# Optimization experiments

Hardware: AMD Instinct MI355X
Metric: run time of the kernel (lower is better)

Reference implementation:

```python
import jax, jax.numpy as jnp
import numpy as np

B, L, T = 256, 1024, 128

def setup_inputs() -> dict:
    key = jax.random.key(0)
    k1, k2, k3, k4 = jax.random.split(key, 4)
    inputs = jax.random.normal(k1, (B, L, T), dtype=jnp.float32)
    tag_indices = jax.random.randint(k2, (B, L), 0, T, dtype=jnp.int64)
    sequence_lengths = jax.random.randint(k3, (B,), 1, L + 1, dtype=jnp.int64)
    # xavier-ish scale for transitions
    transition_params = jax.random.normal(k4, (T, T), dtype=jnp.float32) * (2.0 / (T + T)) ** 0.5
    return {"inputs": inputs, "tag_indices": tag_indices,
            "sequence_lengths": sequence_lengths, "transition_params": transition_params}

def _crf_log_likelihood(inputs, tag_indices, sequence_lengths, transition_params):
    b, l, t = inputs.shape
    mask = (jnp.arange(l)[None, :] < sequence_lengths[:, None]).astype(inputs.dtype)  # [B,L]

    # --- unary score: sum_t inputs[b, t, tag[b,t]] over valid t ---
    unary = jnp.take_along_axis(inputs, tag_indices[:, :, None], axis=2)[:, :, 0]  # [B,L]
    unary_score = jnp.sum(unary * mask, axis=1)

    # --- binary score: sum_t trans[tag[t], tag[t+1]] masked by mask[:,1:] ---
    trans_sc = transition_params[tag_indices[:, :-1], tag_indices[:, 1:]]  # [B,L-1]
    binary_score = jnp.sum(trans_sc * mask[:, 1:], axis=1)
    sequence_scores = unary_score + binary_score

    # --- log normalizer via forward algorithm (log-space scan) ---
    first = inputs[:, 0]                               # [B,T]
    rest = jnp.transpose(inputs[:, 1:], (1, 0, 2))     # [L-1,B,T]

    def step(state, inp_t):
        # state: [B,T] previous alphas; transition broadcast: [B,T_prev,T_next]
        new = inp_t + jax.nn.logsumexp(state[:, :, None] + transition_params[None], axis=1)
        return new, new

    _, alphas = jax.lax.scan(step, first, rest)        # [L-1,B,T]
    # original indexes all_alphas at max(0, seq_len - 2)
    idx = jnp.clip(sequence_lengths - 2, 0, l - 2)
    final_alphas = alphas[idx, jnp.arange(b)]          # [B,T]
    log_norm = jax.nn.logsumexp(final_alphas, axis=1)
    log_norm = jnp.where(sequence_lengths <= 0, jnp.zeros_like(log_norm), log_norm)

    return sequence_scores - log_norm

def reference(inputs, tag_indices, sequence_lengths, transition_params):
    return _crf_log_likelihood(inputs, tag_indices, sequence_lengths, transition_params)
```

## Files before the change

kernel.cpp:

```cpp
#include <hip/hip_runtime.h>


#define B_   256
#define LL   1024
#define TT   128
#define NBLK 16
#define L2E  1.4426950408889634f
#define LN2f 0.6931471805599453f

typedef __attribute__((ext_vector_type(8))) short bf16x8;
typedef __attribute__((ext_vector_type(4))) float f32x4;
union bfrw { unsigned w[4]; bf16x8 v; };

__device__ __forceinline__ unsigned bfround(float x) {
    unsigned u = __float_as_uint(x);
    return u + 0x7fffu + ((u >> 16) & 1u);
}
__device__ __forceinline__ unsigned pack2(float lo, float hi) {
#if __has_builtin(__builtin_amdgcn_cvt_pk_bf16_f32)
    auto p = __builtin_amdgcn_cvt_pk_bf16_f32(lo, hi);
    unsigned w; __builtin_memcpy(&w, &p, 4); return w;
#else
    return __builtin_amdgcn_perm(bfround(hi), bfround(lo), 0x07060302);
#endif
}
__device__ __forceinline__ void lds_barrier() {
    asm volatile("s_waitcnt lgkmcnt(0)\n\ts_barrier" ::: "memory");
}

template<bool FWD, int PH>
__device__ __forceinline__ void phase(int t, float& Dacc, float4 (&up)[4][2],
                                      const bf16x8 (&af)[2][4],
                                      short* qls, float* sb, const float* pu,
                                      float* __restrict__ qcap, float* __restrict__ rcap,
                                      float* __restrict__ dqv, float* __restrict__ drv,
                                      int cb, int tfin, int rank,
                                      int wid, int quad, int bl)
{
    constexpr int CUR  = PH & 1;
    constexpr int NXT  = CUR ^ 1;
    constexpr int SLOT = FWD ? ((1 + PH) & 3) : ((3 - PH) & 3);

    bfrw bfr[4];
    #pragma unroll
    for (int c = 0; c < 4; ++c)
        bfr[c].v = *(const bf16x8*)(qls + CUR * (16 * 136) + bl * 136 + (4 * c + quad) * 8);
    float sprev = sb[CUR * 16 + bl];
    float ci = __builtin_amdgcn_rcpf(sprev);

    f32x4 ae0 = {0.f,0.f,0.f,0.f}, ao0 = {0.f,0.f,0.f,0.f};
    f32x4 ae1 = {0.f,0.f,0.f,0.f}, ao1 = {0.f,0.f,0.f,0.f};
    ae0 = __builtin_amdgcn_mfma_f32_16x16x32_bf16(af[0][0], bfr[0].v, ae0, 0, 0, 0);
    ae1 = __builtin_amdgcn_mfma_f32_16x16x32_bf16(af[1][0], bfr[0].v, ae1, 0, 0, 0);
    ao0 = __builtin_amdgcn_mfma_f32_16x16x32_bf16(af[0][1], bfr[1].v, ao0, 0, 0, 0);
    ao1 = __builtin_amdgcn_mfma_f32_16x16x32_bf16(af[1][1], bfr[1].v, ao1, 0, 0, 0);
    ae0 = __builtin_amdgcn_mfma_f32_16x16x32_bf16(af[0][2], bfr[2].v, ae0, 0, 0, 0);
    ae1 = __builtin_amdgcn_mfma_f32_16x16x32_bf16(af[1][2], bfr[2].v, ae1, 0, 0, 0);
    ao0 = __builtin_amdgcn_mfma_f32_16x16x32_bf16(af[0][3], bfr[3].v, ao0, 0, 0, 0);
    ao1 = __builtin_amdgcn_mfma_f32_16x16x32_bf16(af[1][3], bfr[3].v, ao1, 0, 0, 0);

    float ex[8];
    #pragma unroll
    for (int mt = 0; mt < 2; ++mt) {
        float4 v = up[SLOT][mt];
        ex[4*mt+0] = __builtin_amdgcn_exp2f(v.x * L2E);
        ex[4*mt+1] = __builtin_amdgcn_exp2f(v.y * L2E);
        ex[4*mt+2] = __builtin_amdgcn_exp2f(v.z * L2E);
        ex[4*mt+3] = __builtin_amdgcn_exp2f(v.w * L2E);
    }
    {
        int tp = FWD ? (t + 4) : (t - 5);
        tp = tp < 0 ? 0 : (tp > LL - 1 ? LL - 1 : tp);
        #pragma unroll
        for (int mt = 0; mt < 2; ++mt)
            up[SLOT][mt] = *(const float4*)(pu + (size_t)tp * TT + mt * 16);
    }
    Dacc += __builtin_amdgcn_logf(sprev);

    f32x4 s0v = ae0 + ao0;
    f32x4 s1v = ae1 + ao1;

    float rv[8];
    #pragma unroll
    for (int r = 0; r < 4; ++r) { rv[r] = ci * s0v[r]; rv[4 + r] = ci * s1v[r]; }

    if (!FWD) {
        bool cap = (cb == t - 1) && (cb != tfin);
        if (__any(cap)) {
            if (cap) {
                float4 c0 = {rv[0], rv[1], rv[2], rv[3]};
                float4 c1 = {rv[4], rv[5], rv[6], rv[7]};
                *(float4*)(rcap + rank * TT + wid * 32 + quad * 4) = c0;
                *(float4*)(rcap + rank * TT + wid * 32 + 16 + quad * 4) = c1;
                if (wid == 0 && quad == 0) drv[rank] = Dacc;
            }
        }
        bool inj = (tfin == t - 1);
        #pragma unroll
        for (int k = 0; k < 8; ++k) rv[k] = inj ? 1.0f : rv[k];
        Dacc = inj ? 0.0f : Dacc;
    }

    float ov[8];
    #pragma unroll
    for (int k = 0; k < 8; ++k) ov[k] = ex[k] * rv[k];

    if (FWD) {
        bool cap = (cb == t);
        if (__any(cap)) {
            if (cap) {
                float4 c0 = {ov[0], ov[1], ov[2], ov[3]};
                float4 c1 = {ov[4], ov[5], ov[6], ov[7]};
                *(float4*)(qcap + rank * TT + wid * 32 + quad * 4) = c0;
                *(float4*)(qcap + rank * TT + wid * 32 + 16 + quad * 4) = c1;
                if (wid == 0 && quad == 0) dqv[rank] = Dacc;
            }
        }
    }

    if (wid == 0 && quad == 0) sb[NXT * 16 + bl] = s0v[0];

    bfrw pk;
    pk.w[0] = pack2(ov[0], ov[1]);
    pk.w[1] = pack2(ov[2], ov[3]);
    pk.w[2] = pack2(ov[4], ov[5]);
    pk.w[3] = pack2(ov[6], ov[7]);
    *(bf16x8*)(qls + NXT * (16 * 136) + bl * 136 + (4 * wid + quad) * 8) = pk.v;

    lds_barrier();
}

__launch_bounds__(256, 1)
__global__ void crf_scan(const float* __restrict__ inputs,
                         const int*   __restrict__ tags,
                         const int*   __restrict__ slens,
                         const float* __restrict__ trans,
                         float* __restrict__ qcap, float* __restrict__ rcap,
                         float* __restrict__ dqv,  float* __restrict__ drv,
                         int* __restrict__ perm, float* __restrict__ scorebuf)
{
    __shared__ __align__(16) short qls[2 * 16 * 136];
    __shared__ float sb[2 * 16];
    __shared__ int keys[B_];

    const int tid  = threadIdx.x;

    if (blockIdx.x >= 2 * NBLK) {
        const int sbid = blockIdx.x - 2 * NBLK;
        const int lane = tid & 63, wid = tid >> 6;
        #pragma unroll 1
        for (int bi = 0; bi < 4; ++bi) {
            const int b = sbid * 4 + bi;
            const int slen = slens[b];
            const float* inb  = inputs + (size_t)b * LL * TT;
            const int*   tagb = tags + b * LL;
            float sc = 0.f;
            for (int t = tid; t < slen; t += 256) {
                int tg = tagb[t];
                float v = inb[(size_t)t * TT + tg];
                if (t >= 1) v += trans[tagb[t - 1] * TT + tg];
                sc += v;
            }
            #pragma unroll
            for (int off = 32; off > 0; off >>= 1) sc += __shfl_xor(sc, off, 64);
            if (lane == 0) sb[wid] = sc;
            __syncthreads();
            if (tid == 0) scorebuf[b] = sb[0] + sb[1] + sb[2] + sb[3];
            __syncthreads();
        }
        return;
    }

    const int lane = tid & 63;
    const int wid  = __builtin_amdgcn_readfirstlane(tid >> 6);
    const int quad = lane >> 4;
    const int bl   = lane & 15;
    const bool isf = (blockIdx.x < NBLK);
    const int g    = isf ? blockIdx.x : blockIdx.x - NBLK;

    keys[tid] = slens[tid] * 256 + tid;
    __syncthreads();
    for (int k = 2; k <= B_; k <<= 1) {
        for (int s = k >> 1; s > 0; s >>= 1) {
            int ixj = tid ^ s;
            if (ixj > tid) {
                int a = keys[tid], b2 = keys[ixj];
                bool asc = ((tid & k) == 0);
                if ((a > b2) == asc) { keys[tid] = b2; keys[ixj] = a; }
            }
            __syncthreads();
        }
    }
    if (isf && tid < 16) perm[g * 16 + tid] = keys[g * 16 + tid] & 255;

    const int key = keys[g * 16 + bl];
    const int ob  = key & 255;
    const int sl  = key >> 8;
    int tfin = sl - 1; if (tfin < 1) tfin = 1;

    int tmax = tfin;
    #pragma unroll
    for (int o = 1; o < 16; o <<= 1) {
        int c2 = __shfl_xor(tmax, o, 16); tmax = c2 > tmax ? c2 : tmax;
    }
    tmax = __builtin_amdgcn_readfirstlane(tmax);

    const int C  = (tmax + 4) >> 1;
    const int cb = tfin < C ? tfin : C;

    int cmax = cb, cmin = cb;
    #pragma unroll
    for (int o = 1; o < 16; o <<= 1) {
        int a = __shfl_xor(cmax, o, 16); cmax = a > cmax ? a : cmax;
        int b2 = __shfl_xor(cmin, o, 16); cmin = b2 < cmin ? b2 : cmin;
    }
    cmax = __builtin_amdgcn_readfirstlane(cmax);
    cmin = __builtin_amdgcn_readfirstlane(cmin);

    bf16x8 af[2][4];
    #pragma unroll
    for (int mt = 0; mt < 2; ++mt) {
        const int j = wid * 32 + mt * 16 + bl;
        #pragma unroll
        for (int c = 0; c < 4; ++c) {
            #pragma unroll
            for (int jj = 0; jj < 8; ++jj) {
                int k = 32 * c + 16 * (jj >> 2) + 4 * quad + (jj & 3);
                int idx = isf ? (k * TT + j) : (j * TT + k);
                float ev = __builtin_amdgcn_exp2f(trans[idx] * L2E);
                af[mt][c][jj] = (short)(bfround(ev) >> 16);
            }
        }
    }

    const float* pu = inputs + (size_t)ob * LL * TT + wid * 32 + quad * 4;
    const int rank = g * 16 + bl;
    float Dacc = 0.f;
    float4 up[4][2];

    if (tid < 16) sb[tid] = 1.0f;

    if (isf) {
        float q0[8];
        #pragma unroll
        for (int mt = 0; mt < 2; ++mt) {
            float4 v = *(const float4*)(pu + mt * 16);
            q0[4*mt+0] = __builtin_amdgcn_exp2f(v.x * L2E);
            q0[4*mt+1] = __builtin_amdgcn_exp2f(v.y * L2E);
            q0[4*mt+2] = __builtin_amdgcn_exp2f(v.z * L2E);
            q0[4*mt+3] = __builtin_amdgcn_exp2f(v.w * L2E);
        }
        bfrw pk;
        pk.w[0] = pack2(q0[0], q0[1]);
        pk.w[1] = pack2(q0[2], q0[3]);
        pk.w[2] = pack2(q0[4], q0[5]);
        pk.w[3] = pack2(q0[6], q0[7]);
        *(bf16x8*)(qls + bl * 136 + (4 * wid + quad) * 8) = pk.v;

        #pragma unroll
        for (int s = 1; s <= 4; ++s) {
            #pragma unroll
            for (int mt = 0; mt < 2; ++mt)
                up[s & 3][mt] = *(const float4*)(pu + (size_t)s * TT + mt * 16);
        }
        __syncthreads();

        for (int tb = 1; tb <= cmax; tb += 4) {
            phase<true,0>(tb+0, Dacc, up, af, qls, sb, pu, qcap, rcap, dqv, drv, cb, tfin, rank, wid, quad, bl);
            phase<true,1>(tb+1, Dacc, up, af, qls, sb, pu, qcap, rcap, dqv, drv, cb, tfin, rank, wid, quad, bl);
            phase<true,2>(tb+2, Dacc, up, af, qls, sb, pu, qcap, rcap, dqv, drv, cb, tfin, rank, wid, quad, bl);
            phase<true,3>(tb+3, Dacc, up, af, qls, sb, pu, qcap, rcap, dqv, drv, cb, tfin, rank, wid, quad, bl);
        }
    } else {
        bfrw pk;
        pk.w[0] = pk.w[1] = pk.w[2] = pk.w[3] = 0x3F803F80u;
        *(bf16x8*)(qls + bl * 136 + (4 * wid + quad) * 8) = pk.v;
        if (cb == tfin) {
            float4 one4 = {1.f, 1.f, 1.f, 1.f};
            *(float4*)(rcap + rank * TT + wid * 32 + quad * 4) = one4;
            *(float4*)(rcap + rank * TT + wid * 32 + 16 + quad * 4) = one4;
            if (wid == 0 && quad == 0) drv[rank] = 0.f;
        }

        const int tb0 = (tmax + 4) & ~3;
        #pragma unroll
        for (int ph = 0; ph < 4; ++ph) {
            int ui = tb0 - 1 - ph;
            ui = ui > LL - 1 ? LL - 1 : (ui < 0 ? 0 : ui);
            #pragma unroll
            for (int mt = 0; mt < 2; ++mt)
                up[(3 - ph) & 3][mt] = *(const float4*)(pu + (size_t)ui * TT + mt * 16);
        }
        __syncthreads();

        for (int tb = tb0; tb > cmin; tb -= 4) {
            phase<false,0>(tb-0, Dacc, up, af, qls, sb, pu, qcap, rcap, dqv, drv, cb, tfin, rank, wid, quad, bl);
            phase<false,1>(tb-1, Dacc, up, af, qls, sb, pu, qcap, rcap, dqv, drv, cb, tfin, rank, wid, quad, bl);
            phase<false,2>(tb-2, Dacc, up, af, qls, sb, pu, qcap, rcap, dqv, drv, cb, tfin, rank, wid, quad, bl);
            phase<false,3>(tb-3, Dacc, up, af, qls, sb, pu, qcap, rcap, dqv, drv, cb, tfin, rank, wid, quad, bl);
        }
    }
}

__global__ void crf_comb(const float* __restrict__ qcap, const float* __restrict__ rcap,
                         const float* __restrict__ dqv, const float* __restrict__ drv,
                         const int* __restrict__ perm, const float* __restrict__ scorebuf,
                         float* __restrict__ out) {
    const int tid = threadIdx.x;
    const int r16 = tid >> 4, part = tid & 15;
    const int rank = blockIdx.x * 16 + r16;
    const float* qc = qcap + rank * TT + part * 8;
    const float* rc = rcap + rank * TT + part * 8;
    float4 a0 = *(const float4*)(qc);
    float4 a1 = *(const float4*)(qc + 4);
    float4 b0 = *(const float4*)(rc);
    float4 b1 = *(const float4*)(rc + 4);
    float s = a0.x*b0.x + a0.y*b0.y + a0.z*b0.z + a0.w*b0.w
            + a1.x*b1.x + a1.y*b1.y + a1.z*b1.z + a1.w*b1.w;
    #pragma unroll
    for (int o = 1; o < 16; o <<= 1) s += __shfl_xor(s, o, 16);
    if (part == 0) {
        int ob = perm[rank];
        float logZ = LN2f * (__builtin_amdgcn_logf(s) + dqv[rank] + drv[rank]);
        out[ob] = scorebuf[ob] - logZ;
    }
}

extern "C" void kernel_launch(void* const* d_in, const int* in_sizes, int n_in,
                              void* d_out, int out_size, void* d_ws, size_t ws_size,
                              hipStream_t stream) {
    const float* inputs = (const float*)d_in[0];
    const int*   tags   = (const int*)d_in[1];
    const int*   slens  = (const int*)d_in[2];
    const float* trans  = (const float*)d_in[3];
    float* out = (float*)d_out;

    float* qcap = (float*)d_ws;
    float* rcap = qcap + 32768;
    float* dqv  = rcap + 32768;
    float* drv  = dqv + 256;
    int*   perm = (int*)(drv + 256);
    float* scorebuf = (float*)(perm + 256);

    crf_scan<<<2 * NBLK + 64, 256, 0, stream>>>(inputs, tags, slens, trans,
                                                qcap, rcap, dqv, drv, perm, scorebuf);
    crf_comb<<<NBLK, 256, 0, stream>>>(qcap, rcap, dqv, drv, perm, scorebuf, out);
}
```

Measured before the change: 410.3 us.

## Run each CRF scan block on a single wavefront with register-resident state

Each forward/backward scan block now runs on one 64-lane wavefront instead of four. That wave computes all 128 output tags, using 8 MFMA tiles per K-chunk. The packed bf16 MFMA outputs are fed straight back as the next step's B operand, and the per-sequence scale is broadcast with ds_bpermute. This removes the per-step LDS write/read and the block barrier. In exchange, each wave issues four times as many MFMAs serially and holds much larger register arrays (transition fragments and the prefetch ring). Captured vectors go into LDS and are copied to global memory once at the end.

```diff
diff --git a/kernel.cpp b/kernel.cpp
--- a/kernel.cpp
+++ b/kernel.cpp
@@ -24,110 +24,115 @@
     return __builtin_amdgcn_perm(bfround(hi), bfround(lo), 0x07060302);
 #endif
 }
-__device__ __forceinline__ void lds_barrier() {
-    asm volatile("s_waitcnt lgkmcnt(0)\n\ts_barrier" ::: "memory");
-}
 
 template<bool FWD, int PH>
-__device__ __forceinline__ void phase(int t, float& Dacc, float4 (&up)[4][2],
-                                      const bf16x8 (&af)[2][4],
-                                      short* qls, float* sb, const float* pu,
-                                      float* __restrict__ qcap, float* __restrict__ rcap,
-                                      float* __restrict__ dqv, float* __restrict__ drv,
-                                      int cb, int tfin, int rank,
-                                      int wid, int quad, int bl)
+__device__ __forceinline__ void phase1(int t, float& Dacc, float& sprev,
+                                       float4 (&up)[4][8],
+                                       const bf16x8 (&af)[8][4],
+                                       bf16x8 (&bfr)[4],
+                                       const float* pu,
+                                       float* capl, float* dcap,
+                                       int cb, int tfin, int q, int b)
 {
-    constexpr int CUR  = PH & 1;
-    constexpr int NXT  = CUR ^ 1;
     constexpr int SLOT = FWD ? ((1 + PH) & 3) : ((3 - PH) & 3);
 
-    bfrw bfr[4];
-    #pragma unroll
-    for (int c = 0; c < 4; ++c)
-        bfr[c].v = *(const bf16x8*)(qls + CUR * (16 * 136) + bl * 136 + (4 * c + quad) * 8);
-    float sprev = sb[CUR * 16 + bl];
-    float ci = __builtin_amdgcn_rcpf(sprev);
-
-    f32x4 ae0 = {0.f,0.f,0.f,0.f}, ao0 = {0.f,0.f,0.f,0.f};
-    f32x4 ae1 = {0.f,0.f,0.f,0.f}, ao1 = {0.f,0.f,0.f,0.f};
-    ae0 = __builtin_amdgcn_mfma_f32_16x16x32_bf16(af[0][0], bfr[0].v, ae0, 0, 0, 0);
-    ae1 = __builtin_amdgcn_mfma_f32_16x16x32_bf16(af[1][0], bfr[0].v, ae1, 0, 0, 0);
-    ao0 = __builtin_amdgcn_mfma_f32_16x16x32_bf16(af[0][1], bfr[1].v, ao0, 0, 0, 0);
-    ao1 = __builtin_amdgcn_mfma_f32_16x16x32_bf16(af[1][1], bfr[1].v, ao1, 0, 0, 0);
-    ae0 = __builtin_amdgcn_mfma_f32_16x16x32_bf16(af[0][2], bfr[2].v, ae0, 0, 0, 0);
-    ae1 = __builtin_amdgcn_mfma_f32_16x16x32_bf16(af[1][2], bfr[2].v, ae1, 0, 0, 0);
-    ao0 = __builtin_amdgcn_mfma_f32_16x16x32_bf16(af[0][3], bfr[3].v, ao0, 0, 0, 0);
-    ao1 = __builtin_amdgcn_mfma_f32_16x16x32_bf16(af[1][3], bfr[3].v, ao1, 0, 0, 0);
-
-    float ex[8];
-    #pragma unroll
-    for (int mt = 0; mt < 2; ++mt) {
+    f32x4 acc[8];
+    #pragma unroll
+    for (int mt = 0; mt < 8; ++mt)
+        acc[mt] = __builtin_amdgcn_mfma_f32_16x16x32_bf16(
+            af[mt][0], bfr[0], (f32x4){0.f, 0.f, 0.f, 0.f}, 0, 0, 0);
+    #pragma unroll
+    for (int c = 1; c < 4; ++c) {
+        #pragma unroll
+        for (int mt = 0; mt < 8; ++mt)
+            acc[mt] = __builtin_amdgcn_mfma_f32_16x16x32_bf16(
+                af[mt][c], bfr[c], acc[mt], 0, 0, 0);
+    }
+
+    float ex[8][4];
+    #pragma unroll
+    for (int mt = 0; mt < 8; ++mt) {
         float4 v = up[SLOT][mt];
-        ex[4*mt+0] = __builtin_amdgcn_exp2f(v.x * L2E);
-        ex[4*mt+1] = __builtin_amdgcn_exp2f(v.y * L2E);
-        ex[4*mt+2] = __builtin_amdgcn_exp2f(v.z * L2E);
-        ex[4*mt+3] = __builtin_amdgcn_exp2f(v.w * L2E);
+        ex[mt][0] = __builtin_amdgcn_exp2f(v.x * L2E);
+        ex[mt][1] = __builtin_amdgcn_exp2f(v.y * L2E);
+        ex[mt][2] = __builtin_amdgcn_exp2f(v.z * L2E);
+        ex[mt][3] = __builtin_amdgcn_exp2f(v.w * L2E);
     }
     {
         int tp = FWD ? (t + 4) : (t - 5);
         tp = tp < 0 ? 0 : (tp > LL - 1 ? LL - 1 : tp);
-        #pragma unroll
-        for (int mt = 0; mt < 2; ++mt)
-            up[SLOT][mt] = *(const float4*)(pu + (size_t)tp * TT + mt * 16);
-    }
-    Dacc += __builtin_amdgcn_logf(sprev);
-
-    f32x4 s0v = ae0 + ao0;
-    f32x4 s1v = ae1 + ao1;
-
-    float rv[8];
-    #pragma unroll
-    for (int r = 0; r < 4; ++r) { rv[r] = ci * s0v[r]; rv[4 + r] = ci * s1v[r]; }
+        const float* pt = pu + (size_t)tp * TT;
+        #pragma unroll
+        for (int mt = 0; mt < 8; ++mt)
+            up[SLOT][mt] = *(const float4*)(pt + mt * 16);
+    }
+
+    float ci = __builtin_amdgcn_rcpf(sprev);
+    float lg = __builtin_amdgcn_logf(sprev);
+    bool inj = (!FWD) && (tfin == t - 1);
+    float cis  = inj ? 0.f : ci;
+    float injf = inj ? 1.f : 0.f;
+    Dacc = inj ? 0.f : (Dacc + lg);
+
+    float rv[8][4];
+    #pragma unroll
+    for (int mt = 0; mt < 8; ++mt) {
+        #pragma unroll
+        for (int r = 0; r < 4; ++r)
+            rv[mt][r] = cis * acc[mt][r] + injf;
+    }
 
     if (!FWD) {
         bool cap = (cb == t - 1) && (cb != tfin);
         if (__any(cap)) {
             if (cap) {
-                float4 c0 = {rv[0], rv[1], rv[2], rv[3]};
-                float4 c1 = {rv[4], rv[5], rv[6], rv[7]};
-                *(float4*)(rcap + rank * TT + wid * 32 + quad * 4) = c0;
-                *(float4*)(rcap + rank * TT + wid * 32 + 16 + quad * 4) = c1;
-                if (wid == 0 && quad == 0) drv[rank] = Dacc;
-            }
-        }
-        bool inj = (tfin == t - 1);
-        #pragma unroll
-        for (int k = 0; k < 8; ++k) rv[k] = inj ? 1.0f : rv[k];
-        Dacc = inj ? 0.0f : Dacc;
-    }
-
-    float ov[8];
-    #pragma unroll
-    for (int k = 0; k < 8; ++k) ov[k] = ex[k] * rv[k];
+                #pragma unroll
+                for (int mt = 0; mt < 8; ++mt) {
+                    float4 c4 = {rv[mt][0], rv[mt][1], rv[mt][2], rv[mt][3]};
+                    *(float4*)(capl + b * TT + mt * 16 + q * 4) = c4;
+                }
+                if (q == 0) dcap[b] = Dacc;
+            }
+        }
+    }
+
+    float ov[8][4];
+    #pragma unroll
+    for (int mt = 0; mt < 8; ++mt) {
+        #pragma unroll
+        for (int r = 0; r < 4; ++r)
+            ov[mt][r] = ex[mt][r] * rv[mt][r];
+    }
 
     if (FWD) {
         bool cap = (cb == t);
         if (__any(cap)) {
             if (cap) {
-                float4 c0 = {ov[0], ov[1], ov[2], ov[3]};
-                float4 c1 = {ov[4], ov[5], ov[6], ov[7]};
-                *(float4*)(qcap + rank * TT + wid * 32 + quad * 4) = c0;
-                *(float4*)(qcap + rank * TT + wid * 32 + 16 + quad * 4) = c1;
-                if (wid == 0 && quad == 0) dqv[rank] = Dacc;
-            }
-        }
-    }
-
-    if (wid == 0 && quad == 0) sb[NXT * 16 + bl] = s0v[0];
-
-    bfrw pk;
-    pk.w[0] = pack2(ov[0], ov[1]);
-    pk.w[1] = pack2(ov[2], ov[3]);
-    pk.w[2] = pack2(ov[4], ov[5]);
-    pk.w[3] = pack2(ov[6], ov[7]);
-    *(bf16x8*)(qls + NXT * (16 * 136) + bl * 136 + (4 * wid + quad) * 8) = pk.v;
-
-    lds_barrier();
+                #pragma unroll
+                for (int mt = 0; mt < 8; ++mt) {
+                    float4 c4 = {ov[mt][0], ov[mt][1], ov[mt][2], ov[mt][3]};
+                    *(float4*)(capl + b * TT + mt * 16 + q * 4) = c4;
+                }
+                if (q == 0) dcap[b] = Dacc;
+            }
+        }
+    }
+
+    {
+        int s0i = __float_as_int(acc[0][0]);
+        int sp  = __builtin_amdgcn_ds_bpermute(b << 2, s0i);
+        sprev = __int_as_float(sp);
+    }
+
+    #pragma unroll
+    for (int c = 0; c < 4; ++c) {
+        bfrw pk;
+        pk.w[0] = pack2(ov[2*c][0],     ov[2*c][1]);
+        pk.w[1] = pack2(ov[2*c][2],     ov[2*c][3]);
+        pk.w[2] = pack2(ov[2*c+1][0],   ov[2*c+1][1]);
+        pk.w[3] = pack2(ov[2*c+1][2],   ov[2*c+1][3]);
+        bfr[c] = pk.v;
+    }
 }
 
 __launch_bounds__(256, 1)
@@ -139,11 +144,12 @@
                          float* __restrict__ dqv,  float* __restrict__ drv,
                          int* __restrict__ perm, float* __restrict__ scorebuf)
 {
-    __shared__ __align__(16) short qls[2 * 16 * 136];
+    __shared__ __align__(16) float capl[16 * TT];
+    __shared__ float dcap[16];
     __shared__ float sb[2 * 16];
     __shared__ int keys[B_];
 
-    const int tid  = threadIdx.x;
+    const int tid = threadIdx.x;
 
     if (blockIdx.x >= 2 * NBLK) {
         const int sbid = blockIdx.x - 2 * NBLK;
@@ -171,13 +177,6 @@
         return;
     }
 
-    const int lane = tid & 63;
-    const int wid  = __builtin_amdgcn_readfirstlane(tid >> 6);
-    const int quad = lane >> 4;
-    const int bl   = lane & 15;
-    const bool isf = (blockIdx.x < NBLK);
-    const int g    = isf ? blockIdx.x : blockIdx.x - NBLK;
-
     keys[tid] = slens[tid] * 256 + tid;
     __syncthreads();
     for (int k = 2; k <= B_; k <<= 1) {
@@ -191,9 +190,17 @@
             __syncthreads();
         }
     }
+
+    const bool isf = (blockIdx.x < NBLK);
+    const int g    = isf ? blockIdx.x : blockIdx.x - NBLK;
     if (isf && tid < 16) perm[g * 16 + tid] = keys[g * 16 + tid] & 255;
 
-    const int key = keys[g * 16 + bl];
+    if (tid >= 64) return;
+
+    const int q = tid >> 4;
+    const int b = tid & 15;
+
+    const int key = keys[g * 16 + b];
     const int ob  = key & 255;
     const int sl  = key >> 8;
     int tfin = sl - 1; if (tfin < 1) tfin = 1;
@@ -217,15 +224,15 @@
     cmax = __builtin_amdgcn_readfirstlane(cmax);
     cmin = __builtin_amdgcn_readfirstlane(cmin);
 
-    bf16x8 af[2][4];
-    #pragma unroll
-    for (int mt = 0; mt < 2; ++mt) {
-        const int j = wid * 32 + mt * 16 + bl;
+    bf16x8 af[8][4];
+    #pragma unroll
+    for (int mt = 0; mt < 8; ++mt) {
+        const int j = 16 * mt + b;
         #pragma unroll
         for (int c = 0; c < 4; ++c) {
             #pragma unroll
             for (int jj = 0; jj < 8; ++jj) {
-                int k = 32 * c + 16 * (jj >> 2) + 4 * quad + (jj & 3);
+                int k = 32 * c + 16 * (jj >> 2) + 4 * q + (jj & 3);
                 int idx = isf ? (k * TT + j) : (j * TT + k);
                 float ev = __builtin_amdgcn_exp2f(trans[idx] * L2E);
                 af[mt][c][jj] = (short)(bfround(ev) >> 16);
@@ -233,53 +240,57 @@
         }
     }
 
-    const float* pu = inputs + (size_t)ob * LL * TT + wid * 32 + quad * 4;
-    const int rank = g * 16 + bl;
-    float Dacc = 0.f;
-    float4 up[4][2];
-
-    if (tid < 16) sb[tid] = 1.0f;
+    const float* pu = inputs + (size_t)ob * LL * TT + q * 4;
+    float Dacc = 0.f, sprev = 1.0f;
+    float4 up[4][8];
+    bf16x8 bfr[4];
 
     if (isf) {
-        float q0[8];
-        #pragma unroll
-        for (int mt = 0; mt < 2; ++mt) {
+        float q0[8][4];
+        #pragma unroll
+        for (int mt = 0; mt < 8; ++mt) {
             float4 v = *(const float4*)(pu + mt * 16);
-            q0[4*mt+0] = __builtin_amdgcn_exp2f(v.x * L2E);
-            q0[4*mt+1] = __builtin_amdgcn_exp2f(v.y * L2E);
-            q0[4*mt+2] = __builtin_amdgcn_exp2f(v.z * L2E);
-            q0[4*mt+3] = __builtin_amdgcn_exp2f(v.w * L2E);
-        }
-        bfrw pk;
-        pk.w[0] = pack2(q0[0], q0[1]);
-        pk.w[1] = pack2(q0[2], q0[3]);
-        pk.w[2] = pack2(q0[4], q0[5]);
-        pk.w[3] = pack2(q0[6], q0[7]);
-        *(bf16x8*)(qls + bl * 136 + (4 * wid + quad) * 8) = pk.v;
-
+            q0[mt][0] = __builtin_amdgcn_exp2f(v.x * L2E);
+            q0[mt][1] = __builtin_amdgcn_exp2f(v.y * L2E);
+            q0[mt][2] = __builtin_amdgcn_exp2f(v.z * L2E);
+            q0[mt][3] = __builtin_amdgcn_exp2f(v.w * L2E);
+        }
+        #pragma unroll
+        for (int c = 0; c < 4; ++c) {
+            bfrw pk;
+            pk.w[0] = pack2(q0[2*c][0],   q0[2*c][1]);
+            pk.w[1] = pack2(q0[2*c][2],   q0[2*c][3]);
+            pk.w[2] = pack2(q0[2*c+1][0], q0[2*c+1][1]);
+            pk.w[3] = pack2(q0[2*c+1][2], q0[2*c+1][3]);
+            bfr[c] = pk.v;
+        }
         #pragma unroll
         for (int s = 1; s <= 4; ++s) {
-            #pragma unroll
-            for (int mt = 0; mt < 2; ++mt)
-                up[s & 3][mt] = *(const float4*)(pu + (size_t)s * TT + mt * 16);
-        }
-        __syncthreads();
+            int tp = s > LL - 1 ? LL - 1 : s;
+            #pragma unroll
+            for (int mt = 0; mt < 8; ++mt)
+                up[s & 3][mt] = *(const float4*)(pu + (size_t)tp * TT + mt * 16);
+        }
 
         for (int tb = 1; tb <= cmax; tb += 4) {
-            phase<true,0>(tb+0, Dacc, up, af, qls, sb, pu, qcap, rcap, dqv, drv, cb, tfin, rank, wid, quad, bl);
-            phase<true,1>(tb+1, Dacc, up, af, qls, sb, pu, qcap, rcap, dqv, drv, cb, tfin, rank, wid, quad, bl);
-            phase<true,2>(tb+2, Dacc, up, af, qls, sb, pu, qcap, rcap, dqv, drv, cb, tfin, rank, wid, quad, bl);
-            phase<true,3>(tb+3, Dacc, up, af, qls, sb, pu, qcap, rcap, dqv, drv, cb, tfin, rank, wid, quad, bl);
+            phase1<true,0>(tb+0, Dacc, sprev, up, af, bfr, pu, capl, dcap, cb, tfin, q, b);
+            phase1<true,1>(tb+1, Dacc, sprev, up, af, bfr, pu, capl, dcap, cb, tfin, q, b);
+            phase1<true,2>(tb+2, Dacc, sprev, up, af, bfr, pu, capl, dcap, cb, tfin, q, b);
+            phase1<true,3>(tb+3, Dacc, sprev, up, af, bfr, pu, capl, dcap, cb, tfin, q, b);
         }
     } else {
-        bfrw pk;
-        pk.w[0] = pk.w[1] = pk.w[2] = pk.w[3] = 0x3F803F80u;
-        *(bf16x8*)(qls + bl * 136 + (4 * wid + quad) * 8) = pk.v;
+        {
+            bfrw pk;
+            pk.w[0] = pk.w[1] = pk.w[2] = pk.w[3] = 0x3F803F80u;
+            #pragma unroll
+            for (int c = 0; c < 4; ++c) bfr[c] = pk.v;
+        }
         if (cb == tfin) {
             float4 one4 = {1.f, 1.f, 1.f, 1.f};
-            *(float4*)(rcap + rank * TT + wid * 32 + quad * 4) = one4;
-            *(float4*)(rcap + rank * TT + wid * 32 + 16 + quad * 4) = one4;
-            if (wid == 0 && quad == 0) drv[rank] = 0.f;
+            #pragma unroll
+            for (int mt = 0; mt < 8; ++mt)
+                *(float4*)(capl + b * TT + mt * 16 + q * 4) = one4;
+            if (q == 0) dcap[b] = 0.f;
         }
 
         const int tb0 = (tmax + 4) & ~3;
@@ -288,18 +299,26 @@
             int ui = tb0 - 1 - ph;
             ui = ui > LL - 1 ? LL - 1 : (ui < 0 ? 0 : ui);
             #pragma unroll
-            for (int mt = 0; mt < 2; ++mt)
+            for (int mt = 0; mt < 8; ++mt)
                 up[(3 - ph) & 3][mt] = *(const float4*)(pu + (size_t)ui * TT + mt * 16);
         }
-        __syncthreads();
 
         for (int tb = tb0; tb > cmin; tb -= 4) {
-            phase<false,0>(tb-0, Dacc, up, af, qls, sb, pu, qcap, rcap, dqv, drv, cb, tfin, rank, wid, quad, bl);
-            phase<false,1>(tb-1, Dacc, up, af, qls, sb, pu, qcap, rcap, dqv, drv, cb, tfin, rank, wid, quad, bl);
-            phase<false,2>(tb-2, Dacc, up, af, qls, sb, pu, qcap, rcap, dqv, drv, cb, tfin, rank, wid, quad, bl);
-            phase<false,3>(tb-3, Dacc, up, af, qls, sb, pu, qcap, rcap, dqv, drv, cb, tfin, rank, wid, quad, bl);
-        }
-    }
+            phase1<false,0>(tb-0, Dacc, sprev, up, af, bfr, pu, capl, dcap, cb, tfin, q, b);
+            phase1<false,1>(tb-1, Dacc, sprev, up, af, bfr, pu, capl, dcap, cb, tfin, q, b);
+            phase1<false,2>(tb-2, Dacc, sprev, up, af, bfr, pu, capl, dcap, cb, tfin, q, b);
+            phase1<false,3>(tb-3, Dacc, sprev, up, af, bfr, pu, capl, dcap, cb, tfin, q, b);
+        }
+    }
+
+    asm volatile("s_waitcnt lgkmcnt(0)" ::: "memory");
+    float* gout = isf ? qcap : rcap;
+    #pragma unroll
+    for (int i = 0; i < 8; ++i) {
+        float4 v = *(const float4*)(capl + i * 256 + tid * 4);
+        *(float4*)(gout + (size_t)g * 16 * TT + i * 256 + tid * 4) = v;
+    }
+    if (tid < 16) (isf ? dqv : drv)[g * 16 + tid] = dcap[tid];
 }
 
 __global__ void crf_comb(const float* __restrict__ qcap, const float* __restrict__ rcap,
```

After: 612.1 us. 1.49x slower.

## Merge forward and backward scans into one 512-thread block with register-reused fragments

Applied to the files above, without the earlier changes.

Forward and backward chains for the same 16 sequences now run in one 512-thread block, each half with its own LDS buffers, which halves the scan grid. Each wave keeps its own bf16 B-fragment in registers and reads only the other three from LDS in a fragment-major layout, cutting LDS traffic per step. Captures are staged in LDS and written out at the end, and the backward injection branch becomes arithmetic. Both halves loop for the larger of the two trip counts and share block barriers, so the shorter direction does extra steps.

```diff
diff --git a/kernel.cpp b/kernel.cpp
--- a/kernel.cpp
+++ b/kernel.cpp
@@ -28,109 +28,118 @@
     asm volatile("s_waitcnt lgkmcnt(0)\n\ts_barrier" ::: "memory");
 }
 
+
 template<bool FWD, int PH>
-__device__ __forceinline__ void phase(int t, float& Dacc, float4 (&up)[4][2],
+__device__ __forceinline__ void phase(int t, float& Dacc,
+                                      float4 (&up)[4][2],
                                       const bf16x8 (&af)[2][4],
-                                      short* qls, float* sb, const float* pu,
-                                      float* __restrict__ qcap, float* __restrict__ rcap,
-                                      float* __restrict__ dqv, float* __restrict__ drv,
-                                      int cb, int tfin, int rank,
-                                      int wid, int quad, int bl)
+                                      bf16x8& bs,
+                                      short* fset, float* sb2,
+                                      const float* pu,
+                                      float* cl, float* dc,
+                                      int o0, int o1, int o2, int ws,
+                                      int cb, int tfin, int W4, int q, int b)
 {
     constexpr int CUR  = PH & 1;
     constexpr int NXT  = CUR ^ 1;
     constexpr int SLOT = FWD ? ((1 + PH) & 3) : ((3 - PH) & 3);
 
-    bfrw bfr[4];
-    #pragma unroll
-    for (int c = 0; c < 4; ++c)
-        bfr[c].v = *(const bf16x8*)(qls + CUR * (16 * 136) + bl * 136 + (4 * c + quad) * 8);
-    float sprev = sb[CUR * 16 + bl];
-    float ci = __builtin_amdgcn_rcpf(sprev);
-
-    f32x4 ae0 = {0.f,0.f,0.f,0.f}, ao0 = {0.f,0.f,0.f,0.f};
-    f32x4 ae1 = {0.f,0.f,0.f,0.f}, ao1 = {0.f,0.f,0.f,0.f};
-    ae0 = __builtin_amdgcn_mfma_f32_16x16x32_bf16(af[0][0], bfr[0].v, ae0, 0, 0, 0);
-    ae1 = __builtin_amdgcn_mfma_f32_16x16x32_bf16(af[1][0], bfr[0].v, ae1, 0, 0, 0);
-    ao0 = __builtin_amdgcn_mfma_f32_16x16x32_bf16(af[0][1], bfr[1].v, ao0, 0, 0, 0);
-    ao1 = __builtin_amdgcn_mfma_f32_16x16x32_bf16(af[1][1], bfr[1].v, ao1, 0, 0, 0);
-    ae0 = __builtin_amdgcn_mfma_f32_16x16x32_bf16(af[0][2], bfr[2].v, ae0, 0, 0, 0);
-    ae1 = __builtin_amdgcn_mfma_f32_16x16x32_bf16(af[1][2], bfr[2].v, ae1, 0, 0, 0);
-    ao0 = __builtin_amdgcn_mfma_f32_16x16x32_bf16(af[0][3], bfr[3].v, ao0, 0, 0, 0);
-    ao1 = __builtin_amdgcn_mfma_f32_16x16x32_bf16(af[1][3], bfr[3].v, ao1, 0, 0, 0);
-
-    float ex[8];
-    #pragma unroll
-    for (int mt = 0; mt < 2; ++mt) {
-        float4 v = up[SLOT][mt];
-        ex[4*mt+0] = __builtin_amdgcn_exp2f(v.x * L2E);
-        ex[4*mt+1] = __builtin_amdgcn_exp2f(v.y * L2E);
-        ex[4*mt+2] = __builtin_amdgcn_exp2f(v.z * L2E);
-        ex[4*mt+3] = __builtin_amdgcn_exp2f(v.w * L2E);
+    bf16x8 bo0 = *(const bf16x8*)(fset + CUR * 2048 + o0);
+    bf16x8 bo1 = *(const bf16x8*)(fset + CUR * 2048 + o1);
+    bf16x8 bo2 = *(const bf16x8*)(fset + CUR * 2048 + o2);
+    float sprev = sb2[CUR * 16 + b];
+
+    f32x4 ae0, ae1, ao0, ao1;
+    ae0 = __builtin_amdgcn_mfma_f32_16x16x32_bf16(af[0][0], bs,  (f32x4){0.f,0.f,0.f,0.f}, 0, 0, 0);
+    ae1 = __builtin_amdgcn_mfma_f32_16x16x32_bf16(af[1][0], bs,  (f32x4){0.f,0.f,0.f,0.f}, 0, 0, 0);
+    ao0 = __builtin_amdgcn_mfma_f32_16x16x32_bf16(af[0][1], bo0, (f32x4){0.f,0.f,0.f,0.f}, 0, 0, 0);
+    ao1 = __builtin_amdgcn_mfma_f32_16x16x32_bf16(af[1][1], bo0, (f32x4){0.f,0.f,0.f,0.f}, 0, 0, 0);
+    ae0 = __builtin_amdgcn_mfma_f32_16x16x32_bf16(af[0][2], bo1, ae0, 0, 0, 0);
+    ae1 = __builtin_amdgcn_mfma_f32_16x16x32_bf16(af[1][2], bo1, ae1, 0, 0, 0);
+    ao0 = __builtin_amdgcn_mfma_f32_16x16x32_bf16(af[0][3], bo2, ao0, 0, 0, 0);
+    ao1 = __builtin_amdgcn_mfma_f32_16x16x32_bf16(af[1][3], bo2, ao1, 0, 0, 0);
+
+    float ex[2][4];
+    #pragma unroll
+    for (int m = 0; m < 2; ++m) {
+        float4 v = up[SLOT][m];
+        ex[m][0] = __builtin_amdgcn_exp2f(v.x * L2E);
+        ex[m][1] = __builtin_amdgcn_exp2f(v.y * L2E);
+        ex[m][2] = __builtin_amdgcn_exp2f(v.z * L2E);
+        ex[m][3] = __builtin_amdgcn_exp2f(v.w * L2E);
     }
     {
         int tp = FWD ? (t + 4) : (t - 5);
         tp = tp < 0 ? 0 : (tp > LL - 1 ? LL - 1 : tp);
-        #pragma unroll
-        for (int mt = 0; mt < 2; ++mt)
-            up[SLOT][mt] = *(const float4*)(pu + (size_t)tp * TT + mt * 16);
-    }
-    Dacc += __builtin_amdgcn_logf(sprev);
-
-    f32x4 s0v = ae0 + ao0;
-    f32x4 s1v = ae1 + ao1;
-
-    float rv[8];
-    #pragma unroll
-    for (int r = 0; r < 4; ++r) { rv[r] = ci * s0v[r]; rv[4 + r] = ci * s1v[r]; }
+        const float* pt = pu + (size_t)tp * TT;
+        up[SLOT][0] = *(const float4*)(pt);
+        up[SLOT][1] = *(const float4*)(pt + 16);
+    }
+
+    float ci = __builtin_amdgcn_rcpf(sprev);
+    float lg = __builtin_amdgcn_logf(sprev);
+    bool inj = (!FWD) && (tfin == t - 1);
+    float cis  = inj ? 0.f : ci;
+    float injf = inj ? 1.f : 0.f;
+    Dacc = inj ? 0.f : (Dacc + lg);
+
+    f32x4 a0 = ae0 + ao0;
+    f32x4 a1 = ae1 + ao1;
+
+    float rv[2][4];
+    #pragma unroll
+    for (int r = 0; r < 4; ++r) {
+        rv[0][r] = cis * a0[r] + injf;
+        rv[1][r] = cis * a1[r] + injf;
+    }
 
     if (!FWD) {
         bool cap = (cb == t - 1) && (cb != tfin);
         if (__any(cap)) {
             if (cap) {
-                float4 c0 = {rv[0], rv[1], rv[2], rv[3]};
-                float4 c1 = {rv[4], rv[5], rv[6], rv[7]};
-                *(float4*)(rcap + rank * TT + wid * 32 + quad * 4) = c0;
-                *(float4*)(rcap + rank * TT + wid * 32 + 16 + quad * 4) = c1;
-                if (wid == 0 && quad == 0) drv[rank] = Dacc;
-            }
-        }
-        bool inj = (tfin == t - 1);
-        #pragma unroll
-        for (int k = 0; k < 8; ++k) rv[k] = inj ? 1.0f : rv[k];
-        Dacc = inj ? 0.0f : Dacc;
-    }
-
-    float ov[8];
-    #pragma unroll
-    for (int k = 0; k < 8; ++k) ov[k] = ex[k] * rv[k];
+                float4 c0 = {rv[0][0], rv[0][1], rv[0][2], rv[0][3]};
+                float4 c1 = {rv[1][0], rv[1][1], rv[1][2], rv[1][3]};
+                *(float4*)(cl + b * TT + 32 * W4 + q * 4)      = c0;
+                *(float4*)(cl + b * TT + 32 * W4 + 16 + q * 4) = c1;
+                if (W4 == 0 && q == 0) dc[b] = Dacc;
+            }
+        }
+    }
+
+    float ov[2][4];
+    #pragma unroll
+    for (int r = 0; r < 4; ++r) {
+        ov[0][r] = ex[0][r] * rv[0][r];
+        ov[1][r] = ex[1][r] * rv[1][r];
+    }
 
     if (FWD) {
         bool cap = (cb == t);
         if (__any(cap)) {
             if (cap) {
-                float4 c0 = {ov[0], ov[1], ov[2], ov[3]};
-                float4 c1 = {ov[4], ov[5], ov[6], ov[7]};
-                *(float4*)(qcap + rank * TT + wid * 32 + quad * 4) = c0;
-                *(float4*)(qcap + rank * TT + wid * 32 + 16 + quad * 4) = c1;
-                if (wid == 0 && quad == 0) dqv[rank] = Dacc;
-            }
-        }
-    }
-
-    if (wid == 0 && quad == 0) sb[NXT * 16 + bl] = s0v[0];
+                float4 c0 = {ov[0][0], ov[0][1], ov[0][2], ov[0][3]};
+                float4 c1 = {ov[1][0], ov[1][1], ov[1][2], ov[1][3]};
+                *(float4*)(cl + b * TT + 32 * W4 + q * 4)      = c0;
+                *(float4*)(cl + b * TT + 32 * W4 + 16 + q * 4) = c1;
+                if (W4 == 0 && q == 0) dc[b] = Dacc;
+            }
+        }
+    }
+
+    if (W4 == 0 && q == 0) sb2[NXT * 16 + b] = a0[0];
 
     bfrw pk;
-    pk.w[0] = pack2(ov[0], ov[1]);
-    pk.w[1] = pack2(ov[2], ov[3]);
-    pk.w[2] = pack2(ov[4], ov[5]);
-    pk.w[3] = pack2(ov[6], ov[7]);
-    *(bf16x8*)(qls + NXT * (16 * 136) + bl * 136 + (4 * wid + quad) * 8) = pk.v;
+    pk.w[0] = pack2(ov[0][0], ov[0][1]);
+    pk.w[1] = pack2(ov[0][2], ov[0][3]);
+    pk.w[2] = pack2(ov[1][0], ov[1][1]);
+    pk.w[3] = pack2(ov[1][2], ov[1][3]);
+    bs = pk.v;
+    *(bf16x8*)(fset + NXT * 2048 + ws) = pk.v;
 
     lds_barrier();
 }
 
-__launch_bounds__(256, 1)
+__launch_bounds__(512, 1)
 __global__ void crf_scan(const float* __restrict__ inputs,
                          const int*   __restrict__ tags,
                          const int*   __restrict__ slens,
@@ -139,15 +148,18 @@
                          float* __restrict__ dqv,  float* __restrict__ drv,
                          int* __restrict__ perm, float* __restrict__ scorebuf)
 {
-    __shared__ __align__(16) short qls[2 * 16 * 136];
-    __shared__ float sb[2 * 16];
+    __shared__ __align__(16) short fragls[2][2][4][64 * 8];
+    __shared__ __align__(16) float capl[2][16][TT];
+    __shared__ float dcap[2][16];
+    __shared__ float sbuf[2][2][16];
+    __shared__ float ssb[8];
     __shared__ int keys[B_];
 
-    const int tid  = threadIdx.x;
-
-    if (blockIdx.x >= 2 * NBLK) {
-        const int sbid = blockIdx.x - 2 * NBLK;
-        const int lane = tid & 63, wid = tid >> 6;
+    const int tid = threadIdx.x;
+
+    if (blockIdx.x >= NBLK) {
+        const int sbid = blockIdx.x - NBLK;
+        const int lane = tid & 63, w = tid >> 6;
         #pragma unroll 1
         for (int bi = 0; bi < 4; ++bi) {
             const int b = sbid * 4 + bi;
@@ -155,7 +167,7 @@
             const float* inb  = inputs + (size_t)b * LL * TT;
             const int*   tagb = tags + b * LL;
             float sc = 0.f;
-            for (int t = tid; t < slen; t += 256) {
+            for (int t = tid; t < slen; t += 512) {
                 int tg = tagb[t];
                 float v = inb[(size_t)t * TT + tg];
                 if (t >= 1) v += trans[tagb[t - 1] * TT + tg];
@@ -163,37 +175,42 @@
             }
             #pragma unroll
             for (int off = 32; off > 0; off >>= 1) sc += __shfl_xor(sc, off, 64);
-            if (lane == 0) sb[wid] = sc;
+            if (lane == 0) ssb[w] = sc;
             __syncthreads();
-            if (tid == 0) scorebuf[b] = sb[0] + sb[1] + sb[2] + sb[3];
+            if (tid == 0) scorebuf[b] = ssb[0] + ssb[1] + ssb[2] + ssb[3]
+                                      + ssb[4] + ssb[5] + ssb[6] + ssb[7];
             __syncthreads();
         }
         return;
     }
 
-    const int lane = tid & 63;
-    const int wid  = __builtin_amdgcn_readfirstlane(tid >> 6);
-    const int quad = lane >> 4;
-    const int bl   = lane & 15;
-    const bool isf = (blockIdx.x < NBLK);
-    const int g    = isf ? blockIdx.x : blockIdx.x - NBLK;
-
-    keys[tid] = slens[tid] * 256 + tid;
+    const int g = blockIdx.x;
+
+    if (tid < 256) keys[tid] = slens[tid] * 256 + tid;
     __syncthreads();
     for (int k = 2; k <= B_; k <<= 1) {
         for (int s = k >> 1; s > 0; s >>= 1) {
-            int ixj = tid ^ s;
-            if (ixj > tid) {
-                int a = keys[tid], b2 = keys[ixj];
-                bool asc = ((tid & k) == 0);
-                if ((a > b2) == asc) { keys[tid] = b2; keys[ixj] = a; }
+            if (tid < 256) {
+                int ixj = tid ^ s;
+                if (ixj > tid) {
+                    int a = keys[tid], b2 = keys[ixj];
+                    bool asc = ((tid & k) == 0);
+                    if ((a > b2) == asc) { keys[tid] = b2; keys[ixj] = a; }
+                }
             }
             __syncthreads();
         }
     }
-    if (isf && tid < 16) perm[g * 16 + tid] = keys[g * 16 + tid] & 255;
-
-    const int key = keys[g * 16 + bl];
+    if (tid < 16) perm[g * 16 + tid] = keys[g * 16 + tid] & 255;
+
+    const int set  = tid >> 8;
+    const bool isf = (set == 0);
+    const int lane = tid & 63;
+    const int W4   = __builtin_amdgcn_readfirstlane((tid >> 6) & 3);
+    const int q    = lane >> 4;
+    const int b    = lane & 15;
+
+    const int key = keys[g * 16 + b];
     const int ob  = key & 255;
     const int sl  = key >> 8;
     int tfin = sl - 1; if (tfin < 1) tfin = 1;
@@ -217,89 +234,118 @@
     cmax = __builtin_amdgcn_readfirstlane(cmax);
     cmin = __builtin_amdgcn_readfirstlane(cmin);
 
+    const int tb0 = (tmax + 4) & ~3;
+    const int nif = (cmax + 3) >> 2;
+    const int nib = (tb0 - cmin + 3) >> 2;
+    const int NS  = nif > nib ? nif : nib;
+
+    const int c1 = (W4 == 0) ? 1 : 0;
+    const int c2 = (W4 <= 1) ? 2 : 1;
+    const int c3 = (W4 <= 2) ? 3 : 2;
+    const int o0 = (c1 * 64 + lane) * 8;
+    const int o1 = (c2 * 64 + lane) * 8;
+    const int o2 = (c3 * 64 + lane) * 8;
+    const int ws = (W4 * 64 + lane) * 8;
+
     bf16x8 af[2][4];
     #pragma unroll
-    for (int mt = 0; mt < 2; ++mt) {
-        const int j = wid * 32 + mt * 16 + bl;
+    for (int m = 0; m < 2; ++m) {
+        const int j = 32 * W4 + 16 * m + b;
         #pragma unroll
-        for (int c = 0; c < 4; ++c) {
+        for (int i = 0; i < 4; ++i) {
+            const int c = (i == 0) ? W4 : (i == 1) ? c1 : (i == 2) ? c2 : c3;
             #pragma unroll
             for (int jj = 0; jj < 8; ++jj) {
-                int k = 32 * c + 16 * (jj >> 2) + 4 * quad + (jj & 3);
+                int k = 32 * c + 16 * (jj >> 2) + 4 * q + (jj & 3);
                 int idx = isf ? (k * TT + j) : (j * TT + k);
                 float ev = __builtin_amdgcn_exp2f(trans[idx] * L2E);
-                af[mt][c][jj] = (short)(bfround(ev) >> 16);
-            }
-        }
-    }
-
-    const float* pu = inputs + (size_t)ob * LL * TT + wid * 32 + quad * 4;
-    const int rank = g * 16 + bl;
+                af[m][i][jj] = (short)(bfround(ev) >> 16);
+            }
+        }
+    }
+
+    short* fset = &fragls[set][0][0][0];
+    float* sb2  = &sbuf[set][0][0];
+    float* cl   = &capl[set][0][0];
+    float* dc   = &dcap[set][0];
+
+    const float* pu = inputs + (size_t)ob * LL * TT + 32 * W4 + q * 4;
     float Dacc = 0.f;
     float4 up[4][2];
-
-    if (tid < 16) sb[tid] = 1.0f;
+    bf16x8 bs;
+
+    if (W4 == 0 && lane < 16) sb2[lane] = 1.0f;
 
     if (isf) {
-        float q0[8];
+        float q0[2][4];
         #pragma unroll
-        for (int mt = 0; mt < 2; ++mt) {
-            float4 v = *(const float4*)(pu + mt * 16);
-            q0[4*mt+0] = __builtin_amdgcn_exp2f(v.x * L2E);
-            q0[4*mt+1] = __builtin_amdgcn_exp2f(v.y * L2E);
-            q0[4*mt+2] = __builtin_amdgcn_exp2f(v.z * L2E);
-            q0[4*mt+3] = __builtin_amdgcn_exp2f(v.w * L2E);
+        for (int m = 0; m < 2; ++m) {
+            float4 v = *(const float4*)(pu + m * 16);
+            q0[m][0] = __builtin_amdgcn_exp2f(v.x * L2E);
+            q0[m][1] = __builtin_amdgcn_exp2f(v.y * L2E);
+            q0[m][2] = __builtin_amdgcn_exp2f(v.z * L2E);
+            q0[m][3] = __builtin_amdgcn_exp2f(v.w * L2E);
         }
         bfrw pk;
-        pk.w[0] = pack2(q0[0], q0[1]);
-        pk.w[1] = pack2(q0[2], q0[3]);
-        pk.w[2] = pack2(q0[4], q0[5]);
-        pk.w[3] = pack2(q0[6], q0[7]);
-        *(bf16x8*)(qls + bl * 136 + (4 * wid + quad) * 8) = pk.v;
+        pk.w[0] = pack2(q0[0][0], q0[0][1]);
+        pk.w[1] = pack2(q0[0][2], q0[0][3]);
+        pk.w[2] = pack2(q0[1][0], q0[1][1]);
+        pk.w[3] = pack2(q0[1][2], q0[1][3]);
+        bs = pk.v;
+        *(bf16x8*)(fset + ws) = pk.v;
 
         #pragma unroll
         for (int s = 1; s <= 4; ++s) {
-            #pragma unroll
-            for (int mt = 0; mt < 2; ++mt)
-                up[s & 3][mt] = *(const float4*)(pu + (size_t)s * TT + mt * 16);
-        }
-        __syncthreads();
-
-        for (int tb = 1; tb <= cmax; tb += 4) {
-            phase<true,0>(tb+0, Dacc, up, af, qls, sb, pu, qcap, rcap, dqv, drv, cb, tfin, rank, wid, quad, bl);
-            phase<true,1>(tb+1, Dacc, up, af, qls, sb, pu, qcap, rcap, dqv, drv, cb, tfin, rank, wid, quad, bl);
-            phase<true,2>(tb+2, Dacc, up, af, qls, sb, pu, qcap, rcap, dqv, drv, cb, tfin, rank, wid, quad, bl);
-            phase<true,3>(tb+3, Dacc, up, af, qls, sb, pu, qcap, rcap, dqv, drv, cb, tfin, rank, wid, quad, bl);
+            up[s & 3][0] = *(const float4*)(pu + (size_t)s * TT);
+            up[s & 3][1] = *(const float4*)(pu + (size_t)s * TT + 16);
         }
     } else {
         bfrw pk;
         pk.w[0] = pk.w[1] = pk.w[2] = pk.w[3] = 0x3F803F80u;
-        *(bf16x8*)(qls + bl * 136 + (4 * wid + quad) * 8) = pk.v;
+        bs = pk.v;
+        *(bf16x8*)(fset + ws) = pk.v;
         if (cb == tfin) {
             float4 one4 = {1.f, 1.f, 1.f, 1.f};
-            *(float4*)(rcap + rank * TT + wid * 32 + quad * 4) = one4;
-            *(float4*)(rcap + rank * TT + wid * 32 + 16 + quad * 4) = one4;
-            if (wid == 0 && quad == 0) drv[rank] = 0.f;
-        }
-
-        const int tb0 = (tmax + 4) & ~3;
+            *(float4*)(cl + b * TT + 32 * W4 + q * 4)      = one4;
+            *(float4*)(cl + b * TT + 32 * W4 + 16 + q * 4) = one4;
+            if (W4 == 0 && q == 0) dc[b] = 0.f;
+        }
         #pragma unroll
         for (int ph = 0; ph < 4; ++ph) {
             int ui = tb0 - 1 - ph;
             ui = ui > LL - 1 ? LL - 1 : (ui < 0 ? 0 : ui);
-            #pragma unroll
-            for (int mt = 0; mt < 2; ++mt)
-                up[(3 - ph) & 3][mt] = *(const float4*)(pu + (size_t)ui * TT + mt * 16);
-        }
-        __syncthreads();
-
-        for (int tb = tb0; tb > cmin; tb -= 4) {
-            phase<false,0>(tb-0, Dacc, up, af, qls, sb, pu, qcap, rcap, dqv, drv, cb, tfin, rank, wid, quad, bl);
-            phase<false,1>(tb-1, Dacc, up, af, qls, sb, pu, qcap, rcap, dqv, drv, cb, tfin, rank, wid, quad, bl);
-            phase<false,2>(tb-2, Dacc, up, af, qls, sb, pu, qcap, rcap, dqv, drv, cb, tfin, rank, wid, quad, bl);
-            phase<false,3>(tb-3, Dacc, up, af, qls, sb, pu, qcap, rcap, dqv, drv, cb, tfin, rank, wid, quad, bl);
-        }
-    }
+            up[(3 - ph) & 3][0] = *(const float4*)(pu + (size_t)ui * TT);
+            up[(3 - ph) & 3][1] = *(const float4*)(pu + (size_t)ui * TT + 16);
+        }
+    }
+    __syncthreads();
+
+    if (isf) {
+        for (int i = 0; i < NS; ++i) {
+            const int tb = 1 + 4 * i;
+            phase<true,0>(tb+0, Dacc, up, af, bs, fset, sb2, pu, cl, dc, o0,o1,o2,ws, cb, tfin, W4, q, b);
+            phase<true,1>(tb+1, Dacc, up, af, bs, fset, sb2, pu, cl, dc, o0,o1,o2,ws, cb, tfin, W4, q, b);
+            phase<true,2>(tb+2, Dacc, up, af, bs, fset, sb2, pu, cl, dc, o0,o1,o2,ws, cb, tfin, W4, q, b);
+            phase<true,3>(tb+3, Dacc, up, af, bs, fset, sb2, pu, cl, dc, o0,o1,o2,ws, cb, tfin, W4, q, b);
+        }
+    } else {
+        for (int i = 0; i < NS; ++i) {
+            const int tb = tb0 - 4 * i;
+            phase<false,0>(tb-0, Dacc, up, af, bs, fset, sb2, pu, cl, dc, o0,o1,o2,ws, cb, tfin, W4, q, b);
+            phase<false,1>(tb-1, Dacc, up, af, bs, fset, sb2, pu, cl, dc, o0,o1,o2,ws, cb, tfin, W4, q, b);
+            phase<false,2>(tb-2, Dacc, up, af, bs, fset, sb2, pu, cl, dc, o0,o1,o2,ws, cb, tfin, W4, q, b);
+            phase<false,3>(tb-3, Dacc, up, af, bs, fset, sb2, pu, cl, dc, o0,o1,o2,ws, cb, tfin, W4, q, b);
+        }
+    }
+
+    float* gout = isf ? qcap : rcap;
+    const int ltid = tid & 255;
+    #pragma unroll
+    for (int i = 0; i < 2; ++i) {
+        float4 v = *(const float4*)(cl + i * 1024 + ltid * 4);
+        *(float4*)(gout + (size_t)g * 16 * TT + i * 1024 + ltid * 4) = v;
+    }
+    if (ltid < 16) (isf ? dqv : drv)[g * 16 + ltid] = dc[ltid];
 }
 
 __global__ void crf_comb(const float* __restrict__ qcap, const float* __restrict__ rcap,
@@ -342,7 +388,7 @@
     int*   perm = (int*)(drv + 256);
     float* scorebuf = (float*)(perm + 256);
 
-    crf_scan<<<2 * NBLK + 64, 256, 0, stream>>>(inputs, tags, slens, trans,
-                                                qcap, rcap, dqv, drv, perm, scorebuf);
+    crf_scan<<<NBLK + 64, 512, 0, stream>>>(inputs, tags, slens, trans,
+                                            qcap, rcap, dqv, drv, perm, scorebuf);
     crf_comb<<<NBLK, 256, 0, stream>>>(qcap, rcap, dqv, drv, perm, scorebuf, out);
 }
```

Result: slower. 465.9 us (+13.6%).
